# Kernel optimization log

Hardware: AMD Instinct MI355X
Metric: run time of the kernel (lower is better)

Reference implementation:

```python
import jax, jax.numpy as jnp
import numpy as np

N_NODES = 50000
N_EDGES = 800000
D_IN = 96
D_EDGE = 32
D_OUT = 96
N_TYPES = 4


def setup_inputs() -> dict:
    key = jax.random.key(0)
    k = jax.random.split(key, 6)
    x = jax.random.normal(k[0], (N_NODES, D_IN), dtype=jnp.float32)
    edge_features = jax.random.normal(k[1], (N_NODES, D_EDGE), dtype=jnp.float32)
    edge_index = jax.random.randint(k[2], (2, N_EDGES), 0, N_NODES, dtype=jnp.int32)
    edge_type = jax.random.randint(k[3], (N_EDGES,), 0, N_TYPES, dtype=jnp.int32)
    # One RelEdgeConv per relation type: Linear(D_IN + D_EDGE -> D_OUT) message fn
    scale = 1.0 / np.sqrt(D_IN + D_EDGE)
    W_msg = jax.random.uniform(k[4], (N_TYPES, D_IN + D_EDGE, D_OUT), jnp.float32, -scale, scale)
    b_msg = jax.random.uniform(k[5], (N_TYPES, D_OUT), jnp.float32, -scale, scale)
    return {"x": x, "edge_features": edge_features, "edge_index": edge_index,
            "edge_type": edge_type, "W_msg": W_msg, "b_msg": b_msg}


def reference(x, edge_features, edge_index, edge_type, W_msg, b_msg):
    # Node-level edge_features (shape[0] == N) -> per-edge relative features
    src, dst = edge_index[0], edge_index[1]
    e = jnp.abs(edge_features[src] - edge_features[dst])          # [E, De]
    feat = jnp.concatenate([x[src], e], axis=-1)                  # [E, Din+De]
    n_nodes = x.shape[0]
    n_types = W_msg.shape[0]

    def per_type(t):
        # relation mask: zero out messages for edges of other types
        mask = (edge_type == t).astype(x.dtype)[:, None]          # [E, 1]
        m = (feat @ W_msg[t] + b_msg[t]) * mask                   # [E, Dout]
        # scatter-add messages to destination nodes
        return jax.ops.segment_sum(m, dst, num_segments=n_nodes)  # [N, Dout]

    out = jnp.stack([per_type(t) for t in range(n_types)])        # [T, N, Dout]
    return out.mean(axis=0)
```

## Files before the change

kernel.cpp:

```cpp
#include <hip/hip_runtime.h>

#define E_EDGES 800000
#define NN 50000
#define D_IN 96
#define D_EDGE 32
#define D_OUT 96
#define KSUM 512
#define SSTRIDE 520
#define NB4 3125
#define ECAP 20
#define NBINS 782
#define BINCAP 1280
#define SCATA 400
#define CHUNK 2000
#define CHIT 8
#define BUILD_BLOCKS 512

typedef __attribute__((ext_vector_type(8))) __bf16 bf16x8;
typedef __attribute__((ext_vector_type(4))) float floatx4;

__device__ __forceinline__ float lo16(unsigned int u) {
    return __builtin_bit_cast(float, u << 16);
}
__device__ __forceinline__ float hi16(unsigned int u) {
    return __builtin_bit_cast(float, u & 0xFFFF0000u);
}
__device__ __forceinline__ unsigned int pk2(float a, float b) {
    unsigned short ua = __builtin_bit_cast(unsigned short, (__bf16)a);
    unsigned short ub = __builtin_bit_cast(unsigned short, (__bf16)b);
    return (unsigned int)ua | ((unsigned int)ub << 16);
}

__global__ __launch_bounds__(256) void k_prep(const int* __restrict__ ei,
                                              const int* __restrict__ et,
                                              const float* __restrict__ x,
                                              const float* __restrict__ ef,
                                              const float* __restrict__ Wm,
                                              int* __restrict__ ccnt,
                                              int* __restrict__ CA,
                                              __bf16* __restrict__ WT,
                                              unsigned int* __restrict__ xeb) {
    __shared__ int h[NBINS], base[NBINS], c2[NBINS], gb[NBINS];
    __shared__ uint2 stage[CHUNK];
    int tid = threadIdx.x, bid = blockIdx.x;

    if (bid < SCATA) {
        int e0 = bid * CHUNK;
        for (int i = tid; i < NBINS; i += 256) h[i] = 0;
        __syncthreads();

        unsigned int rec[CHIT];
        int bn[CHIT];
#pragma unroll
        for (int it = 0; it < CHIT; it++) {
            int i = it * 256 + tid;
            bn[it] = -1;
            if (i < CHUNK) {
                int e = e0 + i;
                int dst = ei[E_EDGES + e];
                int ty  = et[e];
                int src = ei[e];
                rec[it] = ((unsigned)src << 8) | ((unsigned)(dst & 63) << 2)
                        | (unsigned)ty;
                int b = dst >> 6;
                bn[it] = b;
                atomicAdd(&h[b], 1);
            }
        }
        __syncthreads();

        if (tid < 64) {
            int lane = tid, carry = 0;
            for (int s = 0; s < NBINS; s += 64) {
                int idx = s + lane;
                int v = (idx < NBINS) ? h[idx] : 0;
                int sc = v;
                for (int d = 1; d < 64; d <<= 1) {
                    int t = __shfl_up(sc, d, 64);
                    if (lane >= d) sc += t;
                }
                if (idx < NBINS) { base[idx] = carry + sc - v; c2[idx] = carry + sc - v; }
                carry += __shfl(sc, 63, 64);
            }
        }
        __syncthreads();

#pragma unroll
        for (int it = 0; it < CHIT; it++) {
            if (bn[it] >= 0) {
                int pos = atomicAdd(&c2[bn[it]], 1);
                stage[pos] = make_uint2(rec[it], (unsigned)bn[it]);
            }
        }
        for (int b = tid; b < NBINS; b += 256)
            gb[b] = h[b] ? atomicAdd(&ccnt[b], h[b]) : 0;
        __syncthreads();

        for (int i = tid; i < CHUNK; i += 256) {
            uint2 s = stage[i];
            int b = (int)s.y;
            int pos = gb[b] + (i - base[b]);
            if (pos < BINCAP) CA[b * BINCAP + pos] = (int)s.x;
        }
    } else {
        int b2 = bid - SCATA;
        int gtid = b2 * 256 + tid;
        int lane = tid & 63, w = tid >> 6;
        for (int n = b2 * 4 + w; n < NN; n += BUILD_BLOCKS * 4) {
            float2 v;
            if (lane < 48) v = *(const float2*)(x  + (size_t)n * D_IN   + 2 * lane);
            else           v = *(const float2*)(ef + (size_t)n * D_EDGE + 2 * (lane - 48));
            xeb[(size_t)n * 64 + lane] = pk2(v.x, v.y);
        }
        for (int i = gtid; i < 96 * KSUM; i += BUILD_BLOCKS * 256) {
            int n = i >> 9, k = i & 511;
            WT[n * KSUM + k] = (__bf16)Wm[(size_t)k * 96 + n];
        }
    }
}

__global__ __launch_bounds__(1024) void k_fused(const int* __restrict__ ccnt,
                                                const int* __restrict__ CA,
                                                const unsigned int* __restrict__ xeb,
                                                const __bf16* __restrict__ WT,
                                                const float* __restrict__ bm,
                                                float* __restrict__ out) {
    __shared__ __align__(16) __bf16 Sl[16][SSTRIDE];
    __shared__ __align__(16) int el[64 * ECAP];
    __shared__ int h[64];

    int tid = threadIdx.x, lane = tid & 63, w = tid >> 6;
    int B = blockIdx.x;
    int b = B >> 2, qtr = B & 3;

    if (tid < 64) h[tid] = 0;
    __syncthreads();

    int m = min(ccnt[b], BINCAP);
    const unsigned int* sp0 = (const unsigned int*)CA + (size_t)b * BINCAP;
    for (int i = tid; i < m; i += 1024) {
        unsigned int r = sp0[i];
        int nl6 = (int)((r >> 2) & 63);
        if ((nl6 >> 4) == qtr) {
            int lk = (nl6 & 15) * 4 + (int)(r & 3);
            int rk = atomicAdd(&h[lk], 1);
            if (rk < ECAP) el[lk * ECAP + rk] = (int)(r >> 8) << 6;
        }
    }
    __syncthreads();
    if (tid < 64) {
        int kc = h[tid];
        int hh = min(kc, ECAP);
        int pp = (hh + 3) & ~3;
        int pv = (B * 16 + (tid >> 2)) << 6;
        for (int rr = hh; rr < pp; rr++) el[tid * ECAP + rr] = pv;
        h[tid] = hh;
    }
    __syncthreads();

    unsigned int Mmask = (lane >= 48) ? 0x7FFFFFFFu : 0xFFFFFFFFu;
    int quad = lane >> 4, low = lane & 15;

#define EDGE(u, sa, sb) do {                                                   \
        float f0 = lo16(u), f1 = hi16(u);                                      \
        f0 = __builtin_bit_cast(float,                                         \
                 __builtin_bit_cast(unsigned int, f0 - e0) & Mmask);           \
        f1 = __builtin_bit_cast(float,                                         \
                 __builtin_bit_cast(unsigned int, f1 - e1) & Mmask);           \
        sa += f0; sb += f1;                                                    \
    } while (0)

    {
        int nl = w;
        int n = B * 16 + nl;
        unsigned int up = xeb[(size_t)n * 64 + lane];
        float xd0 = lo16(up), xd1 = hi16(up);
        float e0 = (lane >= 48) ? xd0 : 0.f;
        float e1 = (lane >= 48) ? xd1 : 0.f;
        float xc0 = (lane < 48) ? xd0 : 0.f;
        float xc1 = (lane < 48) ? xd1 : 0.f;
        unsigned int* sp = (unsigned int*)&Sl[nl][0];

        int h0 = __builtin_amdgcn_readfirstlane(h[nl * 4 + 0]);
        int h1 = __builtin_amdgcn_readfirstlane(h[nl * 4 + 1]);
        int h2 = __builtin_amdgcn_readfirstlane(h[nl * 4 + 2]);
        int h3 = __builtin_amdgcn_readfirstlane(h[nl * 4 + 3]);
        int p0 = (h0 + 3) & ~3, p1 = (h1 + 3) & ~3;
        int p2 = (h2 + 3) & ~3, p3 = (h3 + 3) & ~3;
        const int* q0 = el + nl * 4 * ECAP;
        const int* q1 = q0 + ECAP;
        const int* q2 = q1 + ECAP;
        const int* q3 = q2 + ECAP;

        float sa0 = 0.f, sb0 = 0.f, sa1 = 0.f, sb1 = 0.f;
        float sa2 = 0.f, sb2 = 0.f, sa3 = 0.f, sb3 = 0.f;
        int mx = max(max(p0, p1), max(p2, p3));
        for (int i = 0; i < mx; i += 4) {
            bool o0 = i < p0, o1 = i < p1, o2 = i < p2, o3 = i < p3;
            unsigned int ua0, ua1, ua2, ua3, ub0, ub1, ub2, ub3;
            unsigned int uc0, uc1, uc2, uc3, ue0, ue1, ue2, ue3;
            if (o0) { int4 a = *(const int4*)(q0 + i);
                      ua0 = xeb[a.x + lane]; ua1 = xeb[a.y + lane];
                      ua2 = xeb[a.z + lane]; ua3 = xeb[a.w + lane]; }
            if (o1) { int4 a = *(const int4*)(q1 + i);
                      ub0 = xeb[a.x + lane]; ub1 = xeb[a.y + lane];
                      ub2 = xeb[a.z + lane]; ub3 = xeb[a.w + lane]; }
            if (o2) { int4 a = *(const int4*)(q2 + i);
                      uc0 = xeb[a.x + lane]; uc1 = xeb[a.y + lane];
                      uc2 = xeb[a.z + lane]; uc3 = xeb[a.w + lane]; }
            if (o3) { int4 a = *(const int4*)(q3 + i);
                      ue0 = xeb[a.x + lane]; ue1 = xeb[a.y + lane];
                      ue2 = xeb[a.z + lane]; ue3 = xeb[a.w + lane]; }
            if (o0) { EDGE(ua0, sa0, sb0); EDGE(ua1, sa0, sb0);
                      EDGE(ua2, sa0, sb0); EDGE(ua3, sa0, sb0); }
            if (o1) { EDGE(ub0, sa1, sb1); EDGE(ub1, sa1, sb1);
                      EDGE(ub2, sa1, sb1); EDGE(ub3, sa1, sb1); }
            if (o2) { EDGE(uc0, sa2, sb2); EDGE(uc1, sa2, sb2);
                      EDGE(uc2, sa2, sb2); EDGE(uc3, sa2, sb2); }
            if (o3) { EDGE(ue0, sa3, sb3); EDGE(ue1, sa3, sb3);
                      EDGE(ue2, sa3, sb3); EDGE(ue3, sa3, sb3); }
        }
        sa0 = fmaf((float)(h0 - p0), xc0, sa0); sb0 = fmaf((float)(h0 - p0), xc1, sb0);
        sa1 = fmaf((float)(h1 - p1), xc0, sa1); sb1 = fmaf((float)(h1 - p1), xc1, sb1);
        sa2 = fmaf((float)(h2 - p2), xc0, sa2); sb2 = fmaf((float)(h2 - p2), xc1, sb2);
        sa3 = fmaf((float)(h3 - p3), xc0, sa3); sb3 = fmaf((float)(h3 - p3), xc1, sb3);

        sp[0 * 64 + lane] = pk2(sa0, sb0);
        sp[1 * 64 + lane] = pk2(sa1, sb1);
        sp[2 * 64 + lane] = pk2(sa2, sb2);
        sp[3 * 64 + lane] = pk2(sa3, sb3);
    }
#undef EDGE
    __syncthreads();

    if (w < 6) {
        bf16x8 a[16];
        const __bf16* ap = &Sl[low][0] + quad * 8;
#pragma unroll
        for (int ks = 0; ks < 16; ks++) a[ks] = *(const bf16x8*)(ap + ks * 32);

        int ct = w;
        floatx4 acc = {0.f, 0.f, 0.f, 0.f};
        const __bf16* bp = WT + (size_t)(ct * 16 + low) * KSUM + quad * 8;
#pragma unroll
        for (int ks = 0; ks < 16; ks++)
            acc = __builtin_amdgcn_mfma_f32_16x16x32_bf16(
                a[ks], *(const bf16x8*)(bp + ks * 32), acc, 0, 0, 0);
        int col = ct * 16 + low;
#pragma unroll
        for (int rg = 0; rg < 4; rg++) {
            int r = quad * 4 + rg;
            int g = B * 16 + r;
            float bias = (float)h[r * 4 + 0] * bm[col]
                       + (float)h[r * 4 + 1] * bm[96 + col]
                       + (float)h[r * 4 + 2] * bm[192 + col]
                       + (float)h[r * 4 + 3] * bm[288 + col];
            out[(size_t)g * D_OUT + col] = 0.25f * (acc[rg] + bias);
        }
    }
}

extern "C" void kernel_launch(void* const* d_in, const int* in_sizes, int n_in,
                              void* d_out, int out_size, void* d_ws, size_t ws_size,
                              hipStream_t stream) {
    const float* x  = (const float*)d_in[0];
    const float* ef = (const float*)d_in[1];
    const int*   ei = (const int*)d_in[2];
    const int*   et = (const int*)d_in[3];
    const float* Wm = (const float*)d_in[4];
    const float* bm = (const float*)d_in[5];
    float* out = (float*)d_out;

    int* ccnt = (int*)d_ws;
    int* CA   = ccnt + 1024;
    __bf16* WT  = (__bf16*)(CA + NBINS * BINCAP);
    unsigned int* xeb = (unsigned int*)(WT + 96 * KSUM);

    hipMemsetAsync(ccnt, 0, NBINS * sizeof(int), stream);
    k_prep <<<SCATA + BUILD_BLOCKS, 256, 0, stream>>>(ei, et, x, ef, Wm,
                                                      ccnt, CA, WT, xeb);
    k_fused<<<NB4, 1024, 0, stream>>>(ccnt, CA, xeb, WT, bm, out);
}
```

Baseline: 177.1 us.

## Bin edges per 16-node block directly, dropping staged prefix-scan scatter

The edge binning now uses one bin per 16-destination-node consumer block (3125 bins of capacity 384) instead of 64-node bins that each consumer block rescanned and filtered by quarter. The prep kernel scatters each edge straight to global memory using its local atomic rank plus a global base, removing the shared-memory prefix scan and staging pass. The prep grid is doubled with half-size chunks. The consumer block reads only its own edges, a quarter of what it read before. In exchange the global writes are less coalesced, there are more global atomics on the bin counters, and the smaller bin capacity could drop edges if a bin overflows.

```diff
diff --git a/kernel.cpp b/kernel.cpp
--- a/kernel.cpp
+++ b/kernel.cpp
@@ -9,12 +9,11 @@
 #define SSTRIDE 520
 #define NB4 3125
 #define ECAP 20
-#define NBINS 782
-#define BINCAP 1280
-#define SCATA 400
-#define CHUNK 2000
-#define CHIT 8
-#define BUILD_BLOCKS 512
+#define BCAP 384
+#define SCATA 800
+#define CHUNK 1000
+#define CHIT 4
+#define BUILD_BLOCKS 1024
 
 typedef __attribute__((ext_vector_type(8))) __bf16 bf16x8;
 typedef __attribute__((ext_vector_type(4))) float floatx4;
@@ -40,17 +39,17 @@
                                               int* __restrict__ CA,
                                               __bf16* __restrict__ WT,
                                               unsigned int* __restrict__ xeb) {
-    __shared__ int h[NBINS], base[NBINS], c2[NBINS], gb[NBINS];
-    __shared__ uint2 stage[CHUNK];
+    __shared__ int h[NB4];
+    __shared__ int gb[NB4];
     int tid = threadIdx.x, bid = blockIdx.x;
 
     if (bid < SCATA) {
         int e0 = bid * CHUNK;
-        for (int i = tid; i < NBINS; i += 256) h[i] = 0;
+        for (int i = tid; i < NB4; i += 256) h[i] = 0;
         __syncthreads();
 
         unsigned int rec[CHIT];
-        int bn[CHIT];
+        int rk[CHIT], bn[CHIT];
 #pragma unroll
         for (int it = 0; it < CHIT; it++) {
             int i = it * 256 + tid;
@@ -60,47 +59,22 @@
                 int dst = ei[E_EDGES + e];
                 int ty  = et[e];
                 int src = ei[e];
-                rec[it] = ((unsigned)src << 8) | ((unsigned)(dst & 63) << 2)
+                rec[it] = ((unsigned)src << 6) | ((unsigned)(dst & 15) << 2)
                         | (unsigned)ty;
-                int b = dst >> 6;
-                bn[it] = b;
-                atomicAdd(&h[b], 1);
+                bn[it] = dst >> 4;
+                rk[it] = atomicAdd(&h[bn[it]], 1);
             }
         }
         __syncthreads();
-
-        if (tid < 64) {
-            int lane = tid, carry = 0;
-            for (int s = 0; s < NBINS; s += 64) {
-                int idx = s + lane;
-                int v = (idx < NBINS) ? h[idx] : 0;
-                int sc = v;
-                for (int d = 1; d < 64; d <<= 1) {
-                    int t = __shfl_up(sc, d, 64);
-                    if (lane >= d) sc += t;
-                }
-                if (idx < NBINS) { base[idx] = carry + sc - v; c2[idx] = carry + sc - v; }
-                carry += __shfl(sc, 63, 64);
-            }
-        }
+        for (int b = tid; b < NB4; b += 256)
+            gb[b] = h[b] ? atomicAdd(&ccnt[b], h[b]) : 0;
         __syncthreads();
-
 #pragma unroll
         for (int it = 0; it < CHIT; it++) {
             if (bn[it] >= 0) {
-                int pos = atomicAdd(&c2[bn[it]], 1);
-                stage[pos] = make_uint2(rec[it], (unsigned)bn[it]);
+                int pos = gb[bn[it]] + rk[it];
+                if (pos < BCAP) CA[bn[it] * BCAP + pos] = (int)rec[it];
             }
-        }
-        for (int b = tid; b < NBINS; b += 256)
-            gb[b] = h[b] ? atomicAdd(&ccnt[b], h[b]) : 0;
-        __syncthreads();
-
-        for (int i = tid; i < CHUNK; i += 256) {
-            uint2 s = stage[i];
-            int b = (int)s.y;
-            int pos = gb[b] + (i - base[b]);
-            if (pos < BINCAP) CA[b * BINCAP + pos] = (int)s.x;
         }
     } else {
         int b2 = bid - SCATA;
@@ -131,21 +105,17 @@
 
     int tid = threadIdx.x, lane = tid & 63, w = tid >> 6;
     int B = blockIdx.x;
-    int b = B >> 2, qtr = B & 3;
 
     if (tid < 64) h[tid] = 0;
     __syncthreads();
 
-    int m = min(ccnt[b], BINCAP);
-    const unsigned int* sp0 = (const unsigned int*)CA + (size_t)b * BINCAP;
-    for (int i = tid; i < m; i += 1024) {
-        unsigned int r = sp0[i];
-        int nl6 = (int)((r >> 2) & 63);
-        if ((nl6 >> 4) == qtr) {
-            int lk = (nl6 & 15) * 4 + (int)(r & 3);
-            int rk = atomicAdd(&h[lk], 1);
-            if (rk < ECAP) el[lk * ECAP + rk] = (int)(r >> 8) << 6;
-        }
+    int m = min(ccnt[B], BCAP);
+    const unsigned int* sp0 = (const unsigned int*)CA + (size_t)B * BCAP;
+    if (tid < m) {
+        unsigned int r = sp0[tid];
+        int lk = (int)((r >> 2) & 15) * 4 + (int)(r & 3);
+        int rkk = atomicAdd(&h[lk], 1);
+        if (rkk < ECAP) el[lk * ECAP + rkk] = (int)(r & ~63u);
     }
     __syncthreads();
     if (tid < 64) {
@@ -272,11 +242,11 @@
     float* out = (float*)d_out;
 
     int* ccnt = (int*)d_ws;
-    int* CA   = ccnt + 1024;
-    __bf16* WT  = (__bf16*)(CA + NBINS * BINCAP);
+    int* CA   = ccnt + 3200;
+    __bf16* WT  = (__bf16*)(CA + NB4 * BCAP);
     unsigned int* xeb = (unsigned int*)(WT + 96 * KSUM);
 
-    hipMemsetAsync(ccnt, 0, NBINS * sizeof(int), stream);
+    hipMemsetAsync(ccnt, 0, NB4 * sizeof(int), stream);
     k_prep <<<SCATA + BUILD_BLOCKS, 256, 0, stream>>>(ei, et, x, ef, Wm,
                                                       ccnt, CA, WT, xeb);
     k_fused<<<NB4, 1024, 0, stream>>>(ccnt, CA, xeb, WT, bm, out);
```

Result: slower. 207.2 us (+17.0%).
